# Optimization experiments

Measured on AMD Instinct MI355X. Metric: run time of the kernel, lower is better.

## Reference

```python
import jax, jax.numpy as jnp
import numpy as np


def sparsemax_last(z):
    """Sparsemax over the last axis (Martins & Astudillo 2016)."""
    dims = z.shape[-1]
    z_sorted = jnp.sort(z, axis=-1)[..., ::-1]          # descending
    z_cumsum = jnp.cumsum(z_sorted, axis=-1)
    k = jnp.arange(1, dims + 1, dtype=z.dtype)
    support = 1.0 + k * z_sorted > z_cumsum              # [..., dims] bool
    k_z = jnp.sum(support.astype(jnp.int32), axis=-1)    # support size >= 1 for finite z
    tau_sum = jnp.take_along_axis(z_cumsum, (k_z - 1)[..., None], axis=-1)[..., 0]
    tau = (tau_sum - 1.0) / k_z.astype(z.dtype)
    return jnp.maximum(z - tau[..., None], 0.0)


def _bin_codes_1hot(depth, dtype):
    n_leaf = 2 ** depth
    indices = np.arange(n_leaf)
    offsets = 2 ** np.arange(depth)
    codes = (indices[None, :] // offsets[:, None]) % 2   # [depth, 2^depth]
    onehot = np.stack([codes, 1 - codes], axis=-1)       # [depth, 2^depth, 2]
    return jnp.asarray(onehot, dtype=dtype)


def setup_inputs() -> dict:
    key = jax.random.key(0)
    ks = jax.random.split(key, 5)
    B, I, N, D, U = 1024, 256, 512, 6, 16
    return {
        "x": jax.random.normal(ks[0], (B, I), dtype=jnp.float32),
        "feature_selection_logits": jax.random.normal(ks[1], (I, N, D), dtype=jnp.float32),
        "feature_thresholds": jax.random.normal(ks[2], (N, D), dtype=jnp.float32),
        "log_temperatures": jax.random.normal(ks[3], (N, D), dtype=jnp.float32) * 0.1,
        "response": jax.random.normal(ks[4], (N, U, 2 ** D), dtype=jnp.float32),
    }


def reference(x, feature_selection_logits, feature_thresholds, log_temperatures, response):
    depth = feature_thresholds.shape[1]
    # feature selection via sparsemax over depth axis (axis=-1, as in source)
    feature_selectors = sparsemax_last(feature_selection_logits)          # [I,N,D]
    feature_values = jnp.einsum('bi,ind->bnd', x, feature_selectors)      # [B,N,D]
    # temperature-scaled threshold logits
    tl = (feature_values - feature_thresholds) * jnp.exp(-log_temperatures)
    tl = jnp.stack([-tl, tl], axis=-1)                                    # [B,N,D,2]
    bins = jnp.clip(0.5 * tl + 0.5, 0.0, 1.0)                             # sparsemoid
    onehot = _bin_codes_1hot(depth, bins.dtype)                           # [D,2^D,2]
    bin_matches = jnp.einsum('btds,dcs->btdc', bins, onehot)              # [B,N,D,2^D]
    response_weights = jnp.prod(bin_matches, axis=-2)                     # [B,N,2^D]
    out = jnp.einsum('bnd,ncd->bnc', response_weights, response)          # [B,N,U]
    return jnp.sum(out, axis=1)                                           # [B,U]
```

## Files before the change

kernel.cpp:

```cpp
#include <hip/hip_runtime.h>
#include <hip/hip_bf16.h>

#define B_SZ 1024
#define I_SZ 256
#define N_SZ 512
#define D_SZ 6
#define U_SZ 16
#define C_SZ 64
#define K_SZ (N_SZ * D_SZ)
#define NSPLIT 64

typedef __bf16 bf16_t;
typedef bf16_t bf16x8 __attribute__((ext_vector_type(8)));
typedef bf16_t bf16x4 __attribute__((ext_vector_type(4)));
typedef float  f32x4  __attribute__((ext_vector_type(4)));

__global__ __launch_bounds__(256) void prep_k(
    const float* __restrict__ x, const float* __restrict__ resp,
    const float* __restrict__ lt, const float* __restrict__ fsl,
    bf16_t* __restrict__ xb, bf16_t* __restrict__ respb,
    float* __restrict__ elt, bf16_t* __restrict__ selT) {
  __shared__ float sT[96][17];
  const int bid = blockIdx.x;
  if (bid < 256) {
    const int idx = (bid * 256 + threadIdx.x) * 4;
    const float4 v = *(const float4*)(x + idx);
    bf16x4 o; o[0] = (bf16_t)v.x; o[1] = (bf16_t)v.y; o[2] = (bf16_t)v.z; o[3] = (bf16_t)v.w;
    *(bf16x4*)(xb + idx) = o;
  } else if (bid < 768) {
    const int idx = ((bid - 256) * 256 + threadIdx.x) * 4;
    const float4 v = *(const float4*)(resp + idx);
    bf16x4 o; o[0] = (bf16_t)v.x; o[1] = (bf16_t)v.y; o[2] = (bf16_t)v.z; o[3] = (bf16_t)v.w;
    *(bf16x4*)(respb + idx) = o;
  } else if (bid < 780) {
    const int i = (bid - 768) * 256 + threadIdx.x;
    elt[i] = __expf(-lt[i]);
  } else {
    const int sbid = bid - 780;
    const int t = threadIdx.x;
    const int i_loc = t >> 4, n_loc = t & 15;
    const int n0 = (sbid & 31) * 16, i0 = (sbid >> 5) * 16;

    const float* z = fsl + ((size_t)(i0 + i_loc) * N_SZ + (n0 + n_loc)) * D_SZ;
    float v[D_SZ], s[D_SZ];
#pragma unroll
    for (int d = 0; d < D_SZ; ++d) { v[d] = z[d]; s[d] = v[d]; }

#define CSWAP(a, b) { float hi = fmaxf(s[a], s[b]); float lo = fminf(s[a], s[b]); s[a] = hi; s[b] = lo; }
#pragma unroll
    for (int r = 0; r < 3; ++r) {
      CSWAP(0, 1) CSWAP(2, 3) CSWAP(4, 5)
      CSWAP(1, 2) CSWAP(3, 4)
    }
#undef CSWAP

    float cs[D_SZ];
    cs[0] = s[0];
#pragma unroll
    for (int j = 1; j < D_SZ; ++j) cs[j] = cs[j - 1] + s[j];
    int kz = 0;
#pragma unroll
    for (int j = 0; j < D_SZ; ++j)
      kz += (1.0f + (float)(j + 1) * s[j] > cs[j]) ? 1 : 0;
    const float tau = (cs[kz - 1] - 1.0f) / (float)kz;

#pragma unroll
    for (int d = 0; d < D_SZ; ++d)
      sT[n_loc * 6 + d][i_loc] = fmaxf(v[d] - tau, 0.0f);
    __syncthreads();

    if (t < 192) {
      const int row = t >> 1, half = t & 1;
      bf16x8 o;
#pragma unroll
      for (int jj = 0; jj < 8; ++jj) o[jj] = (bf16_t)sT[row][half * 8 + jj];
      *(bf16x8*)(selT + (size_t)(n0 * 6 + row) * I_SZ + i0 + half * 8) = o;
    }
  }
}

__global__ __launch_bounds__(256) void fused_k(
    const bf16_t* __restrict__ selT,
    const bf16_t* __restrict__ xb,
    const float* __restrict__ th,
    const float* __restrict__ elt,
    const bf16_t* __restrict__ respb,
    float* __restrict__ part) {
  __shared__ float fv[48][68];
  const int lane = threadIdx.x & 63, wave = threadIdx.x >> 6;
  const int lm = lane & 15, q = lane >> 4;
  const int btile = blockIdx.x & 15, ns = blockIdx.x >> 4;

  if (wave < 3) {
    f32x4 acc[4];
#pragma unroll
    for (int s = 0; s < 4; ++s) acc[s] = (f32x4){0.f, 0.f, 0.f, 0.f};
    const bf16_t* arow = selT + (size_t)(ns * 48 + wave * 16 + lm) * I_SZ + q * 8;
    const bf16_t* brow = xb + (size_t)(btile * 64 + lm) * I_SZ + q * 8;
#pragma unroll
    for (int kk = 0; kk < I_SZ; kk += 32) {
      const bf16x8 a = *(const bf16x8*)(arow + kk);
#pragma unroll
      for (int s = 0; s < 4; ++s) {
        const bf16x8 bv = *(const bf16x8*)(brow + (size_t)s * 16 * I_SZ + kk);
        acc[s] = __builtin_amdgcn_mfma_f32_16x16x32_bf16(a, bv, acc[s], 0, 0, 0);
      }
    }
#pragma unroll
    for (int s = 0; s < 4; ++s)
#pragma unroll
      for (int r = 0; r < 4; ++r)
        fv[wave * 16 + q * 4 + r][s * 16 + lm] = acc[s][r];
  }
  __syncthreads();

  f32x4 acc = (f32x4){0.f, 0.f, 0.f, 0.f};
  const int bloc = wave * 16 + lm;

#pragma unroll
  for (int j = 0; j < 8; ++j) {
    const int n = ns * 8 + j;
    float b0v[D_SZ], b1v[D_SZ];
#pragma unroll
    for (int d = 0; d < D_SZ; ++d) {
      const float fvv = fv[j * 6 + d][bloc];
      const float tl  = (fvv - th[n * 6 + d]) * elt[n * 6 + d];
      b1v[d] = fminf(fmaxf(0.5f * tl + 0.5f, 0.0f), 1.0f);
      b0v[d] = fminf(fmaxf(0.5f - 0.5f * tl, 0.0f), 1.0f);
    }
    float p2[2], p4[4], p8[8];
    p2[0] = b1v[0]; p2[1] = b0v[0];
#pragma unroll
    for (int i = 0; i < 4; ++i) p4[i] = p2[i & 1] * ((i & 2) ? b0v[1] : b1v[1]);
#pragma unroll
    for (int i = 0; i < 8; ++i) p8[i] = p4[i & 3] * ((i & 4) ? b0v[2] : b1v[2]);
    const float f3 = (q & 1) ? b0v[3] : b1v[3];
    const float f4 = (q & 2) ? b0v[4] : b1v[4];
    const float fq = f3 * f4;
    const float g0 = fq * b1v[5];
    const float g1 = fq * b0v[5];

    bf16x8 a0, a1;
#pragma unroll
    for (int jj = 0; jj < 8; ++jj) {
      a0[jj] = (bf16_t)(p8[jj] * g0);
      a1[jj] = (bf16_t)(p8[jj] * g1);
    }
    const bf16_t* rb = respb + (size_t)n * (U_SZ * C_SZ) + lm * C_SZ + q * 8;
    const bf16x8 bv0 = *(const bf16x8*)(rb);
    const bf16x8 bv1 = *(const bf16x8*)(rb + 32);
    acc = __builtin_amdgcn_mfma_f32_16x16x32_bf16(a0, bv0, acc, 0, 0, 0);
    acc = __builtin_amdgcn_mfma_f32_16x16x32_bf16(a1, bv1, acc, 0, 0, 0);
  }

#pragma unroll
  for (int r = 0; r < 4; ++r)
    part[(size_t)ns * (B_SZ * U_SZ) +
         (size_t)(btile * 64 + wave * 16 + q * 4 + r) * U_SZ + lm] = acc[r];
}

__global__ __launch_bounds__(256) void reduce_k(
    const float* __restrict__ part, float* __restrict__ out) {
  __shared__ float red[4][64];
  const int t = threadIdx.x;
  const int o = blockIdx.x * 64 + (t & 63);
  const int g = t >> 6;
  float s = 0.0f;
#pragma unroll
  for (int k = 0; k < 16; ++k)
    s += part[(size_t)(g * 16 + k) * (B_SZ * U_SZ) + o];
  red[g][t & 63] = s;
  __syncthreads();
  if (t < 64)
    out[blockIdx.x * 64 + t] = red[0][t] + red[1][t] + red[2][t] + red[3][t];
}

extern "C" void kernel_launch(void* const* d_in, const int* in_sizes, int n_in,
                              void* d_out, int out_size, void* d_ws, size_t ws_size,
                              hipStream_t stream) {
  const float* x    = (const float*)d_in[0];
  const float* fsl  = (const float*)d_in[1];
  const float* th   = (const float*)d_in[2];
  const float* lt   = (const float*)d_in[3];
  const float* resp = (const float*)d_in[4];
  float* out = (float*)d_out;

  char* w = (char*)d_ws;
  bf16_t* xb    = (bf16_t*)(w);
  bf16_t* respb = (bf16_t*)(w + 524288);
  float*  elt   = (float*)(w + 1572864);
  bf16_t* selT  = (bf16_t*)(w + 1585152);
  float*  part  = (float*)(w + 3158016);

  prep_k<<<1292, 256, 0, stream>>>(x, resp, lt, fsl, xb, respb, elt, selT);

  fused_k<<<16 * NSPLIT, 256, 0, stream>>>(selT, xb, th, elt, respb, part);

  reduce_k<<<(B_SZ * U_SZ) / 64, 256, 0, stream>>>(part, out);
}
```

Baseline: 93.48 us.

## Merge prep, fused and reduce kernels into one cooperative kernel with grid syncs

The three separate launches (prep, fused GEMM/response, reduce) become a single cooperative kernel of 1024 blocks that uses grid.sync() between phases. The goal is to remove two kernel launch gaps and the inter-kernel drain. The threshold and temperature scaling also moves into the first-stage epilogue, so the second stage reads the scaled logits directly. In exchange, every block must wait at two grid-wide barriers, the 1292 prep work units are strided over 1024 blocks, and the cooperative launch needs all 1024 blocks to be co-resident.

```diff
diff --git a/kernel.cpp b/kernel.cpp
--- a/kernel.cpp
+++ b/kernel.cpp
@@ -1,5 +1,8 @@
 #include <hip/hip_runtime.h>
 #include <hip/hip_bf16.h>
+#include <hip/hip_cooperative_groups.h>
+
+namespace cg = cooperative_groups;
 
 #define B_SZ 1024
 #define I_SZ 256
@@ -7,7 +10,6 @@
 #define D_SZ 6
 #define U_SZ 16
 #define C_SZ 64
-#define K_SZ (N_SZ * D_SZ)
 #define NSPLIT 64
 
 typedef __bf16 bf16_t;
@@ -15,164 +17,172 @@
 typedef bf16_t bf16x4 __attribute__((ext_vector_type(4)));
 typedef float  f32x4  __attribute__((ext_vector_type(4)));
 
-__global__ __launch_bounds__(256) void prep_k(
-    const float* __restrict__ x, const float* __restrict__ resp,
-    const float* __restrict__ lt, const float* __restrict__ fsl,
+__global__ __launch_bounds__(256, 4) void odst_coop(
+    const float* __restrict__ x, const float* __restrict__ fsl,
+    const float* __restrict__ th, const float* __restrict__ lt,
+    const float* __restrict__ resp,
     bf16_t* __restrict__ xb, bf16_t* __restrict__ respb,
-    float* __restrict__ elt, bf16_t* __restrict__ selT) {
-  __shared__ float sT[96][17];
-  const int bid = blockIdx.x;
-  if (bid < 256) {
-    const int idx = (bid * 256 + threadIdx.x) * 4;
-    const float4 v = *(const float4*)(x + idx);
-    bf16x4 o; o[0] = (bf16_t)v.x; o[1] = (bf16_t)v.y; o[2] = (bf16_t)v.z; o[3] = (bf16_t)v.w;
-    *(bf16x4*)(xb + idx) = o;
-  } else if (bid < 768) {
-    const int idx = ((bid - 256) * 256 + threadIdx.x) * 4;
-    const float4 v = *(const float4*)(resp + idx);
-    bf16x4 o; o[0] = (bf16_t)v.x; o[1] = (bf16_t)v.y; o[2] = (bf16_t)v.z; o[3] = (bf16_t)v.w;
-    *(bf16x4*)(respb + idx) = o;
-  } else if (bid < 780) {
-    const int i = (bid - 768) * 256 + threadIdx.x;
-    elt[i] = __expf(-lt[i]);
-  } else {
-    const int sbid = bid - 780;
-    const int t = threadIdx.x;
-    const int i_loc = t >> 4, n_loc = t & 15;
-    const int n0 = (sbid & 31) * 16, i0 = (sbid >> 5) * 16;
-
-    const float* z = fsl + ((size_t)(i0 + i_loc) * N_SZ + (n0 + n_loc)) * D_SZ;
-    float v[D_SZ], s[D_SZ];
-#pragma unroll
-    for (int d = 0; d < D_SZ; ++d) { v[d] = z[d]; s[d] = v[d]; }
+    float* __restrict__ elt, bf16_t* __restrict__ selT,
+    float* __restrict__ part, float* __restrict__ out) {
+  __shared__ float smem[48 * 68];
+  cg::grid_group grid = cg::this_grid();
+  const int bid = blockIdx.x, t = threadIdx.x;
+
+  for (int u = bid; u < 1292; u += 1024) {
+    if (u < 256) {
+      const int idx = (u * 256 + t) * 4;
+      const float4 v = *(const float4*)(x + idx);
+      bf16x4 o; o[0] = (bf16_t)v.x; o[1] = (bf16_t)v.y; o[2] = (bf16_t)v.z; o[3] = (bf16_t)v.w;
+      *(bf16x4*)(xb + idx) = o;
+    } else if (u < 768) {
+      const int idx = ((u - 256) * 256 + t) * 4;
+      const float4 v = *(const float4*)(resp + idx);
+      bf16x4 o; o[0] = (bf16_t)v.x; o[1] = (bf16_t)v.y; o[2] = (bf16_t)v.z; o[3] = (bf16_t)v.w;
+      *(bf16x4*)(respb + idx) = o;
+    } else if (u < 780) {
+      const int i = (u - 768) * 256 + t;
+      elt[i] = __expf(-lt[i]);
+    } else {
+      float (*sT)[17] = (float(*)[17])smem;
+      const int sbid = u - 780;
+      const int i_loc = t >> 4, n_loc = t & 15;
+      const int n0 = (sbid & 31) * 16, i0 = (sbid >> 5) * 16;
+
+      const float* z = fsl + ((size_t)(i0 + i_loc) * N_SZ + (n0 + n_loc)) * D_SZ;
+      float v[D_SZ], s[D_SZ];
+#pragma unroll
+      for (int d = 0; d < D_SZ; ++d) { v[d] = z[d]; s[d] = v[d]; }
 
 #define CSWAP(a, b) { float hi = fmaxf(s[a], s[b]); float lo = fminf(s[a], s[b]); s[a] = hi; s[b] = lo; }
 #pragma unroll
-    for (int r = 0; r < 3; ++r) {
-      CSWAP(0, 1) CSWAP(2, 3) CSWAP(4, 5)
-      CSWAP(1, 2) CSWAP(3, 4)
-    }
+      for (int r = 0; r < 3; ++r) {
+        CSWAP(0, 1) CSWAP(2, 3) CSWAP(4, 5)
+        CSWAP(1, 2) CSWAP(3, 4)
+      }
 #undef CSWAP
 
-    float cs[D_SZ];
-    cs[0] = s[0];
-#pragma unroll
-    for (int j = 1; j < D_SZ; ++j) cs[j] = cs[j - 1] + s[j];
-    int kz = 0;
-#pragma unroll
-    for (int j = 0; j < D_SZ; ++j)
-      kz += (1.0f + (float)(j + 1) * s[j] > cs[j]) ? 1 : 0;
-    const float tau = (cs[kz - 1] - 1.0f) / (float)kz;
-
-#pragma unroll
-    for (int d = 0; d < D_SZ; ++d)
-      sT[n_loc * 6 + d][i_loc] = fmaxf(v[d] - tau, 0.0f);
-    __syncthreads();
-
-    if (t < 192) {
-      const int row = t >> 1, half = t & 1;
-      bf16x8 o;
-#pragma unroll
-      for (int jj = 0; jj < 8; ++jj) o[jj] = (bf16_t)sT[row][half * 8 + jj];
-      *(bf16x8*)(selT + (size_t)(n0 * 6 + row) * I_SZ + i0 + half * 8) = o;
+      float cs[D_SZ];
+      cs[0] = s[0];
+#pragma unroll
+      for (int j = 1; j < D_SZ; ++j) cs[j] = cs[j - 1] + s[j];
+      int kz = 0;
+#pragma unroll
+      for (int j = 0; j < D_SZ; ++j)
+        kz += (1.0f + (float)(j + 1) * s[j] > cs[j]) ? 1 : 0;
+      const float tau = (cs[kz - 1] - 1.0f) / (float)kz;
+
+#pragma unroll
+      for (int d = 0; d < D_SZ; ++d)
+        sT[n_loc * 6 + d][i_loc] = fmaxf(v[d] - tau, 0.0f);
+      __syncthreads();
+
+      if (t < 192) {
+        const int row = t >> 1, half = t & 1;
+        bf16x8 o;
+#pragma unroll
+        for (int jj = 0; jj < 8; ++jj) o[jj] = (bf16_t)sT[row][half * 8 + jj];
+        *(bf16x8*)(selT + (size_t)(n0 * 6 + row) * I_SZ + i0 + half * 8) = o;
+      }
     }
   }
-}
-
-__global__ __launch_bounds__(256) void fused_k(
-    const bf16_t* __restrict__ selT,
-    const bf16_t* __restrict__ xb,
-    const float* __restrict__ th,
-    const float* __restrict__ elt,
-    const bf16_t* __restrict__ respb,
-    float* __restrict__ part) {
-  __shared__ float fv[48][68];
-  const int lane = threadIdx.x & 63, wave = threadIdx.x >> 6;
-  const int lm = lane & 15, q = lane >> 4;
-  const int btile = blockIdx.x & 15, ns = blockIdx.x >> 4;
-
-  if (wave < 3) {
-    f32x4 acc[4];
-#pragma unroll
-    for (int s = 0; s < 4; ++s) acc[s] = (f32x4){0.f, 0.f, 0.f, 0.f};
-    const bf16_t* arow = selT + (size_t)(ns * 48 + wave * 16 + lm) * I_SZ + q * 8;
-    const bf16_t* brow = xb + (size_t)(btile * 64 + lm) * I_SZ + q * 8;
-#pragma unroll
-    for (int kk = 0; kk < I_SZ; kk += 32) {
-      const bf16x8 a = *(const bf16x8*)(arow + kk);
-#pragma unroll
-      for (int s = 0; s < 4; ++s) {
-        const bf16x8 bv = *(const bf16x8*)(brow + (size_t)s * 16 * I_SZ + kk);
-        acc[s] = __builtin_amdgcn_mfma_f32_16x16x32_bf16(a, bv, acc[s], 0, 0, 0);
-      }
+
+  grid.sync();
+
+  {
+    float (*fv)[68] = (float(*)[68])smem;
+    const int lane = t & 63, wave = t >> 6;
+    const int lm = lane & 15, q = lane >> 4;
+    const int btile = bid & 15, ns = bid >> 4;
+
+    if (wave < 3) {
+      f32x4 acc[4];
+#pragma unroll
+      for (int s = 0; s < 4; ++s) acc[s] = (f32x4){0.f, 0.f, 0.f, 0.f};
+      const bf16_t* arow = selT + (size_t)(ns * 48 + wave * 16 + lm) * I_SZ + q * 8;
+      const bf16_t* brow = xb + (size_t)(btile * 64 + lm) * I_SZ + q * 8;
+#pragma unroll
+      for (int kk = 0; kk < I_SZ; kk += 32) {
+        const bf16x8 a = *(const bf16x8*)(arow + kk);
+#pragma unroll
+        for (int s = 0; s < 4; ++s) {
+          const bf16x8 bv = *(const bf16x8*)(brow + (size_t)s * 16 * I_SZ + kk);
+          acc[s] = __builtin_amdgcn_mfma_f32_16x16x32_bf16(a, bv, acc[s], 0, 0, 0);
+        }
+      }
+      float thv[4], ev[4];
+#pragma unroll
+      for (int r = 0; r < 4; ++r) {
+        const int kp = ns * 48 + wave * 16 + q * 4 + r;
+        thv[r] = th[kp]; ev[r] = elt[kp];
+      }
+#pragma unroll
+      for (int s = 0; s < 4; ++s)
+#pragma unroll
+        for (int r = 0; r < 4; ++r)
+          fv[wave * 16 + q * 4 + r][s * 16 + lm] = (acc[s][r] - thv[r]) * ev[r];
     }
-#pragma unroll
-    for (int s = 0; s < 4; ++s)
-#pragma unroll
-      for (int r = 0; r < 4; ++r)
-        fv[wave * 16 + q * 4 + r][s * 16 + lm] = acc[s][r];
+    __syncthreads();
+
+    f32x4 acc = (f32x4){0.f, 0.f, 0.f, 0.f};
+    const int bloc = wave * 16 + lm;
+
+#pragma unroll
+    for (int j = 0; j < 8; ++j) {
+      const int n = ns * 8 + j;
+      const bf16_t* rb = respb + (size_t)n * (U_SZ * C_SZ) + lm * C_SZ + q * 8;
+      const bf16x8 bv0 = *(const bf16x8*)(rb);
+      const bf16x8 bv1 = *(const bf16x8*)(rb + 32);
+
+      float b0v[D_SZ], b1v[D_SZ];
+#pragma unroll
+      for (int d = 0; d < D_SZ; ++d) {
+        const float tl = fv[j * 6 + d][bloc];
+        b1v[d] = fminf(fmaxf(0.5f * tl + 0.5f, 0.0f), 1.0f);
+        b0v[d] = fminf(fmaxf(0.5f - 0.5f * tl, 0.0f), 1.0f);
+      }
+      float p2[2], p4[4], p8[8];
+      p2[0] = b1v[0]; p2[1] = b0v[0];
+#pragma unroll
+      for (int i = 0; i < 4; ++i) p4[i] = p2[i & 1] * ((i & 2) ? b0v[1] : b1v[1]);
+#pragma unroll
+      for (int i = 0; i < 8; ++i) p8[i] = p4[i & 3] * ((i & 4) ? b0v[2] : b1v[2]);
+      const float f3 = (q & 1) ? b0v[3] : b1v[3];
+      const float f4 = (q & 2) ? b0v[4] : b1v[4];
+      const float fq = f3 * f4;
+      const float g0 = fq * b1v[5];
+      const float g1 = fq * b0v[5];
+
+      bf16x8 a0, a1;
+#pragma unroll
+      for (int jj = 0; jj < 8; ++jj) {
+        a0[jj] = (bf16_t)(p8[jj] * g0);
+        a1[jj] = (bf16_t)(p8[jj] * g1);
+      }
+      acc = __builtin_amdgcn_mfma_f32_16x16x32_bf16(a0, bv0, acc, 0, 0, 0);
+      acc = __builtin_amdgcn_mfma_f32_16x16x32_bf16(a1, bv1, acc, 0, 0, 0);
+    }
+
+#pragma unroll
+    for (int r = 0; r < 4; ++r)
+      part[(size_t)ns * (B_SZ * U_SZ) +
+           (size_t)(btile * 64 + wave * 16 + q * 4 + r) * U_SZ + lm] = acc[r];
   }
-  __syncthreads();
-
-  f32x4 acc = (f32x4){0.f, 0.f, 0.f, 0.f};
-  const int bloc = wave * 16 + lm;
-
-#pragma unroll
-  for (int j = 0; j < 8; ++j) {
-    const int n = ns * 8 + j;
-    float b0v[D_SZ], b1v[D_SZ];
-#pragma unroll
-    for (int d = 0; d < D_SZ; ++d) {
-      const float fvv = fv[j * 6 + d][bloc];
-      const float tl  = (fvv - th[n * 6 + d]) * elt[n * 6 + d];
-      b1v[d] = fminf(fmaxf(0.5f * tl + 0.5f, 0.0f), 1.0f);
-      b0v[d] = fminf(fmaxf(0.5f - 0.5f * tl, 0.0f), 1.0f);
-    }
-    float p2[2], p4[4], p8[8];
-    p2[0] = b1v[0]; p2[1] = b0v[0];
-#pragma unroll
-    for (int i = 0; i < 4; ++i) p4[i] = p2[i & 1] * ((i & 2) ? b0v[1] : b1v[1]);
-#pragma unroll
-    for (int i = 0; i < 8; ++i) p8[i] = p4[i & 3] * ((i & 4) ? b0v[2] : b1v[2]);
-    const float f3 = (q & 1) ? b0v[3] : b1v[3];
-    const float f4 = (q & 2) ? b0v[4] : b1v[4];
-    const float fq = f3 * f4;
-    const float g0 = fq * b1v[5];
-    const float g1 = fq * b0v[5];
-
-    bf16x8 a0, a1;
-#pragma unroll
-    for (int jj = 0; jj < 8; ++jj) {
-      a0[jj] = (bf16_t)(p8[jj] * g0);
-      a1[jj] = (bf16_t)(p8[jj] * g1);
-    }
-    const bf16_t* rb = respb + (size_t)n * (U_SZ * C_SZ) + lm * C_SZ + q * 8;
-    const bf16x8 bv0 = *(const bf16x8*)(rb);
-    const bf16x8 bv1 = *(const bf16x8*)(rb + 32);
-    acc = __builtin_amdgcn_mfma_f32_16x16x32_bf16(a0, bv0, acc, 0, 0, 0);
-    acc = __builtin_amdgcn_mfma_f32_16x16x32_bf16(a1, bv1, acc, 0, 0, 0);
+
+  grid.sync();
+
+  if (bid < 256) {
+    float (*red)[64] = (float(*)[64])smem;
+    const int o = bid * 64 + (t & 63);
+    const int g = t >> 6;
+    float s = 0.0f;
+#pragma unroll
+    for (int k = 0; k < 16; ++k)
+      s += part[(size_t)(g * 16 + k) * (B_SZ * U_SZ) + o];
+    red[g][t & 63] = s;
+    __syncthreads();
+    if (t < 64)
+      out[bid * 64 + t] = red[0][t] + red[1][t] + red[2][t] + red[3][t];
   }
-
-#pragma unroll
-  for (int r = 0; r < 4; ++r)
-    part[(size_t)ns * (B_SZ * U_SZ) +
-         (size_t)(btile * 64 + wave * 16 + q * 4 + r) * U_SZ + lm] = acc[r];
-}
-
-__global__ __launch_bounds__(256) void reduce_k(
-    const float* __restrict__ part, float* __restrict__ out) {
-  __shared__ float red[4][64];
-  const int t = threadIdx.x;
-  const int o = blockIdx.x * 64 + (t & 63);
-  const int g = t >> 6;
-  float s = 0.0f;
-#pragma unroll
-  for (int k = 0; k < 16; ++k)
-    s += part[(size_t)(g * 16 + k) * (B_SZ * U_SZ) + o];
-  red[g][t & 63] = s;
-  __syncthreads();
-  if (t < 64)
-    out[blockIdx.x * 64 + t] = red[0][t] + red[1][t] + red[2][t] + red[3][t];
 }
 
 extern "C" void kernel_launch(void* const* d_in, const int* in_sizes, int n_in,
@@ -192,9 +202,9 @@
   bf16_t* selT  = (bf16_t*)(w + 1585152);
   float*  part  = (float*)(w + 3158016);
 
-  prep_k<<<1292, 256, 0, stream>>>(x, resp, lt, fsl, xb, respb, elt, selT);
-
-  fused_k<<<16 * NSPLIT, 256, 0, stream>>>(selT, xb, th, elt, respb, part);
-
-  reduce_k<<<(B_SZ * U_SZ) / 64, 256, 0, stream>>>(part, out);
+  void* args[] = {(void*)&x, (void*)&fsl, (void*)&th, (void*)&lt, (void*)&resp,
+                  (void*)&xb, (void*)&respb, (void*)&elt, (void*)&selT,
+                  (void*)&part, (void*)&out};
+  hipLaunchCooperativeKernel((void*)odst_coop, dim3(16 * NSPLIT), dim3(256),
+                             args, 0, stream);
 }
```

After: 337.6 us. 3.61x slower.

## Fuse sparsemax and bf16 conversion prep into main kernel, drop prep launch

Applied to the files above, without the earlier changes.

Removes the separate prep kernel. Each block of the main kernel now computes sparsemax for its own 48 selector columns across all 256 inputs into shared memory. It also converts x and response from fp32 to bf16 on the fly and folds the threshold and exp(-log_temp) transform into the first-stage epilogue. This saves one launch and the workspace round trip, but every one of the 16 btile blocks recomputes the same sparsemax slice, and fp32 x is read directly at twice the bytes. Shared memory per block grows, and launch bounds now request 4 blocks per CU.

```diff
diff --git a/kernel.cpp b/kernel.cpp
--- a/kernel.cpp
+++ b/kernel.cpp
@@ -7,110 +7,93 @@
 #define D_SZ 6
 #define U_SZ 16
 #define C_SZ 64
-#define K_SZ (N_SZ * D_SZ)
 #define NSPLIT 64
 
 typedef __bf16 bf16_t;
 typedef bf16_t bf16x8 __attribute__((ext_vector_type(8)));
-typedef bf16_t bf16x4 __attribute__((ext_vector_type(4)));
 typedef float  f32x4  __attribute__((ext_vector_type(4)));
 
-__global__ __launch_bounds__(256) void prep_k(
-    const float* __restrict__ x, const float* __restrict__ resp,
-    const float* __restrict__ lt, const float* __restrict__ fsl,
-    bf16_t* __restrict__ xb, bf16_t* __restrict__ respb,
-    float* __restrict__ elt, bf16_t* __restrict__ selT) {
-  __shared__ float sT[96][17];
-  const int bid = blockIdx.x;
-  if (bid < 256) {
-    const int idx = (bid * 256 + threadIdx.x) * 4;
-    const float4 v = *(const float4*)(x + idx);
-    bf16x4 o; o[0] = (bf16_t)v.x; o[1] = (bf16_t)v.y; o[2] = (bf16_t)v.z; o[3] = (bf16_t)v.w;
-    *(bf16x4*)(xb + idx) = o;
-  } else if (bid < 768) {
-    const int idx = ((bid - 256) * 256 + threadIdx.x) * 4;
-    const float4 v = *(const float4*)(resp + idx);
-    bf16x4 o; o[0] = (bf16_t)v.x; o[1] = (bf16_t)v.y; o[2] = (bf16_t)v.z; o[3] = (bf16_t)v.w;
-    *(bf16x4*)(respb + idx) = o;
-  } else if (bid < 780) {
-    const int i = (bid - 768) * 256 + threadIdx.x;
-    elt[i] = __expf(-lt[i]);
-  } else {
-    const int sbid = bid - 780;
-    const int t = threadIdx.x;
-    const int i_loc = t >> 4, n_loc = t & 15;
-    const int n0 = (sbid & 31) * 16, i0 = (sbid >> 5) * 16;
+#define SEL_P 264
 
-    const float* z = fsl + ((size_t)(i0 + i_loc) * N_SZ + (n0 + n_loc)) * D_SZ;
-    float v[D_SZ], s[D_SZ];
+__global__ __launch_bounds__(256, 4) void fused_k(
+    const float* __restrict__ x,
+    const float* __restrict__ fsl,
+    const float* __restrict__ th,
+    const float* __restrict__ lt,
+    const float* __restrict__ resp,
+    float* __restrict__ part) {
+  __shared__ bf16_t selS[48 * SEL_P];
+  __shared__ float  fv[48][68];
+  const int t = threadIdx.x;
+  const int lane = t & 63, wave = t >> 6;
+  const int lm = lane & 15, q = lane >> 4;
+  const int btile = blockIdx.x & 15, ns = blockIdx.x >> 4;
+
+  {
+    const float* zbase = fsl + (size_t)t * (N_SZ * D_SZ) + ns * 48;
+    float v[48];
 #pragma unroll
-    for (int d = 0; d < D_SZ; ++d) { v[d] = z[d]; s[d] = v[d]; }
+    for (int c = 0; c < 12; ++c) *(float4*)&v[c * 4] = *(const float4*)(zbase + c * 4);
 
+#pragma unroll
+    for (int j = 0; j < 8; ++j) {
+      float* z = v + j * 6;
+      float s[D_SZ];
+#pragma unroll
+      for (int d = 0; d < D_SZ; ++d) s[d] = z[d];
 #define CSWAP(a, b) { float hi = fmaxf(s[a], s[b]); float lo = fminf(s[a], s[b]); s[a] = hi; s[b] = lo; }
 #pragma unroll
-    for (int r = 0; r < 3; ++r) {
-      CSWAP(0, 1) CSWAP(2, 3) CSWAP(4, 5)
-      CSWAP(1, 2) CSWAP(3, 4)
-    }
+      for (int r = 0; r < 3; ++r) {
+        CSWAP(0, 1) CSWAP(2, 3) CSWAP(4, 5)
+        CSWAP(1, 2) CSWAP(3, 4)
+      }
 #undef CSWAP
-
-    float cs[D_SZ];
-    cs[0] = s[0];
+      float cs[D_SZ];
+      cs[0] = s[0];
 #pragma unroll
-    for (int j = 1; j < D_SZ; ++j) cs[j] = cs[j - 1] + s[j];
-    int kz = 0;
+      for (int k = 1; k < D_SZ; ++k) cs[k] = cs[k - 1] + s[k];
+      int kz = 0;
 #pragma unroll
-    for (int j = 0; j < D_SZ; ++j)
-      kz += (1.0f + (float)(j + 1) * s[j] > cs[j]) ? 1 : 0;
-    const float tau = (cs[kz - 1] - 1.0f) / (float)kz;
-
+      for (int k = 0; k < D_SZ; ++k)
+        kz += (1.0f + (float)(k + 1) * s[k] > cs[k]) ? 1 : 0;
+      const float tau = (cs[kz - 1] - 1.0f) / (float)kz;
 #pragma unroll
-    for (int d = 0; d < D_SZ; ++d)
-      sT[n_loc * 6 + d][i_loc] = fmaxf(v[d] - tau, 0.0f);
-    __syncthreads();
-
-    if (t < 192) {
-      const int row = t >> 1, half = t & 1;
-      bf16x8 o;
-#pragma unroll
-      for (int jj = 0; jj < 8; ++jj) o[jj] = (bf16_t)sT[row][half * 8 + jj];
-      *(bf16x8*)(selT + (size_t)(n0 * 6 + row) * I_SZ + i0 + half * 8) = o;
+      for (int d = 0; d < D_SZ; ++d)
+        selS[(j * 6 + d) * SEL_P + t] = (bf16_t)fmaxf(z[d] - tau, 0.0f);
     }
   }
-}
-
-__global__ __launch_bounds__(256) void fused_k(
-    const bf16_t* __restrict__ selT,
-    const bf16_t* __restrict__ xb,
-    const float* __restrict__ th,
-    const float* __restrict__ elt,
-    const bf16_t* __restrict__ respb,
-    float* __restrict__ part) {
-  __shared__ float fv[48][68];
-  const int lane = threadIdx.x & 63, wave = threadIdx.x >> 6;
-  const int lm = lane & 15, q = lane >> 4;
-  const int btile = blockIdx.x & 15, ns = blockIdx.x >> 4;
+  __syncthreads();
 
   if (wave < 3) {
     f32x4 acc[4];
 #pragma unroll
     for (int s = 0; s < 4; ++s) acc[s] = (f32x4){0.f, 0.f, 0.f, 0.f};
-    const bf16_t* arow = selT + (size_t)(ns * 48 + wave * 16 + lm) * I_SZ + q * 8;
-    const bf16_t* brow = xb + (size_t)(btile * 64 + lm) * I_SZ + q * 8;
+    const bf16_t* arow = selS + (wave * 16 + lm) * SEL_P + q * 8;
 #pragma unroll
     for (int kk = 0; kk < I_SZ; kk += 32) {
       const bf16x8 a = *(const bf16x8*)(arow + kk);
 #pragma unroll
       for (int s = 0; s < 4; ++s) {
-        const bf16x8 bv = *(const bf16x8*)(brow + (size_t)s * 16 * I_SZ + kk);
+        const float* xr = x + (size_t)(btile * 64 + s * 16 + lm) * I_SZ + kk + q * 8;
+        const float4 x0 = *(const float4*)(xr);
+        const float4 x1 = *(const float4*)(xr + 4);
+        bf16x8 bv;
+        bv[0] = (bf16_t)x0.x; bv[1] = (bf16_t)x0.y; bv[2] = (bf16_t)x0.z; bv[3] = (bf16_t)x0.w;
+        bv[4] = (bf16_t)x1.x; bv[5] = (bf16_t)x1.y; bv[6] = (bf16_t)x1.z; bv[7] = (bf16_t)x1.w;
         acc[s] = __builtin_amdgcn_mfma_f32_16x16x32_bf16(a, bv, acc[s], 0, 0, 0);
       }
+    }
+    float thv[4], ev[4];
+#pragma unroll
+    for (int r = 0; r < 4; ++r) {
+      const int kp = ns * 48 + wave * 16 + q * 4 + r;
+      thv[r] = th[kp]; ev[r] = __expf(-lt[kp]);
     }
 #pragma unroll
     for (int s = 0; s < 4; ++s)
 #pragma unroll
       for (int r = 0; r < 4; ++r)
-        fv[wave * 16 + q * 4 + r][s * 16 + lm] = acc[s][r];
+        fv[wave * 16 + q * 4 + r][s * 16 + lm] = (acc[s][r] - thv[r]) * ev[r];
   }
   __syncthreads();
 
@@ -120,11 +103,21 @@
 #pragma unroll
   for (int j = 0; j < 8; ++j) {
     const int n = ns * 8 + j;
+    const float* rb = resp + (size_t)n * (U_SZ * C_SZ) + lm * C_SZ + q * 8;
+    const float4 r0 = *(const float4*)(rb);
+    const float4 r1 = *(const float4*)(rb + 4);
+    const float4 r2 = *(const float4*)(rb + 32);
+    const float4 r3 = *(const float4*)(rb + 36);
+    bf16x8 bv0, bv1;
+    bv0[0] = (bf16_t)r0.x; bv0[1] = (bf16_t)r0.y; bv0[2] = (bf16_t)r0.z; bv0[3] = (bf16_t)r0.w;
+    bv0[4] = (bf16_t)r1.x; bv0[5] = (bf16_t)r1.y; bv0[6] = (bf16_t)r1.z; bv0[7] = (bf16_t)r1.w;
+    bv1[0] = (bf16_t)r2.x; bv1[1] = (bf16_t)r2.y; bv1[2] = (bf16_t)r2.z; bv1[3] = (bf16_t)r2.w;
+    bv1[4] = (bf16_t)r3.x; bv1[5] = (bf16_t)r3.y; bv1[6] = (bf16_t)r3.z; bv1[7] = (bf16_t)r3.w;
+
     float b0v[D_SZ], b1v[D_SZ];
 #pragma unroll
     for (int d = 0; d < D_SZ; ++d) {
-      const float fvv = fv[j * 6 + d][bloc];
-      const float tl  = (fvv - th[n * 6 + d]) * elt[n * 6 + d];
+      const float tl = fv[j * 6 + d][bloc];
       b1v[d] = fminf(fmaxf(0.5f * tl + 0.5f, 0.0f), 1.0f);
       b0v[d] = fminf(fmaxf(0.5f - 0.5f * tl, 0.0f), 1.0f);
     }
@@ -146,9 +139,6 @@
       a0[jj] = (bf16_t)(p8[jj] * g0);
       a1[jj] = (bf16_t)(p8[jj] * g1);
     }
-    const bf16_t* rb = respb + (size_t)n * (U_SZ * C_SZ) + lm * C_SZ + q * 8;
-    const bf16x8 bv0 = *(const bf16x8*)(rb);
-    const bf16x8 bv1 = *(const bf16x8*)(rb + 32);
     acc = __builtin_amdgcn_mfma_f32_16x16x32_bf16(a0, bv0, acc, 0, 0, 0);
     acc = __builtin_amdgcn_mfma_f32_16x16x32_bf16(a1, bv1, acc, 0, 0, 0);
   }
@@ -185,16 +175,9 @@
   const float* resp = (const float*)d_in[4];
   float* out = (float*)d_out;
 
-  char* w = (char*)d_ws;
-  bf16_t* xb    = (bf16_t*)(w);
-  bf16_t* respb = (bf16_t*)(w + 524288);
-  float*  elt   = (float*)(w + 1572864);
-  bf16_t* selT  = (bf16_t*)(w + 1585152);
-  float*  part  = (float*)(w + 3158016);
+  float* part = (float*)d_ws;
 
-  prep_k<<<1292, 256, 0, stream>>>(x, resp, lt, fsl, xb, respb, elt, selT);
-
-  fused_k<<<16 * NSPLIT, 256, 0, stream>>>(selT, xb, th, elt, respb, part);
+  fused_k<<<16 * NSPLIT, 256, 0, stream>>>(x, fsl, th, lt, resp, part);
 
   reduce_k<<<(B_SZ * U_SZ) / 64, 256, 0, stream>>>(part, out);
 }
```

New measurement: 109.6 us. 17.2% more time.
